# Kernel optimization log

Measured on AMD Instinct MI355X. Metric: run time of the kernel, lower is better.

## Reference

```python
import jax, jax.numpy as jnp
import numpy as np

B, BOUNDS, NRIM, K, UNITS = 4096, 512, 6, 4, 600
H_IN, DK_IN, DV_IN = 4, 64, 400
H_C, DK_C, DV_C = 4, 32, 100


def setup_inputs() -> dict:
    key = jax.random.key(0)
    ks = jax.random.split(key, 16)
    s = 0.02
    return {
        'inputs': jax.random.normal(ks[0], (B, BOUNDS + NRIM), jnp.float32),
        'hs': jax.random.normal(ks[1], (B, NRIM, UNITS), jnp.float32) * s,
        'cs': jax.random.normal(ks[2], (B, NRIM, UNITS), jnp.float32) * s,
        'Wk': jax.random.normal(ks[3], (BOUNDS, H_IN * DK_IN), jnp.float32) * s,
        'bk': jnp.zeros((H_IN * DK_IN,), jnp.float32),
        'Wv': jax.random.normal(ks[4], (BOUNDS, H_IN * DV_IN), jnp.float32) * s,
        'bv': jnp.zeros((H_IN * DV_IN,), jnp.float32),
        'Wq': jax.random.normal(ks[5], (NRIM, UNITS, H_IN * DK_IN), jnp.float32) * s,
        'lstm_k': jax.random.normal(ks[6], (NRIM, DV_IN, 4 * UNITS), jnp.float32) * s,
        'lstm_r': jax.random.normal(ks[7], (NRIM, UNITS, 4 * UNITS), jnp.float32) * s,
        'lstm_b': jnp.zeros((NRIM, 4 * UNITS), jnp.float32),
        'Wkc': jax.random.normal(ks[8], (NRIM, UNITS, H_C * DK_C), jnp.float32) * s,
        'Wvc': jax.random.normal(ks[9], (NRIM, UNITS, H_C * DV_C), jnp.float32) * s,
        'Wqc': jax.random.normal(ks[10], (NRIM, UNITS, H_C * DK_C), jnp.float32) * s,
        'Wout': jax.random.normal(ks[11], (NRIM, H_C * DV_C, UNITS), jnp.float32) * s,
    }


def _split_heads(t, n_heads, d_head):
    # [B, T, n_heads*d_head] -> [B, n_heads, T, d_head] (matches tf.split+stack)
    b, t_len = t.shape[0], t.shape[1]
    return t.reshape(b, t_len, n_heads, d_head).transpose(0, 2, 1, 3)


def reference(inputs, hs, cs, Wk, bk, Wv, bv, Wq, lstm_k, lstm_r, lstm_b, Wkc, Wvc, Wqc, Wout):
    x = inputs[:, :BOUNDS]                                   # [B, bounds]
    rim_dist = inputs[:, BOUNDS:BOUNDS + NRIM]               # [B, nRIM]

    # ---- input attention ----
    xx = jnp.stack([x, jnp.zeros_like(x)], axis=1)           # [B, 2, bounds]
    k_lay = xx @ Wk + bk                                     # [B, 2, H*dk]
    v_lay = xx @ Wv + bv                                     # [B, 2, H*dv]
    q_lay = jnp.einsum('bnu,nuo->bno', hs, Wq)               # grouped linear [B, nRIM, H*dq]
    kh = _split_heads(k_lay, H_IN, DK_IN)                    # [B, H, 2, dk]
    vh = _split_heads(v_lay, H_IN, DV_IN)                    # [B, H, 2, dv]
    qh = _split_heads(q_lay, H_IN, DK_IN)                    # [B, H, nRIM, dk]
    v2 = vh.mean(axis=1)                                     # [B, 2, dv]
    scores = jnp.einsum('bhnd,bhtd->bhnt', qh, kh) / np.sqrt(DK_IN).astype(np.float32)
    scores2 = scores.mean(axis=1)                            # [B, nRIM, 2]

    # top-k RIM selection mask from RIM_dist (use_attn=False path)
    _, idx = jax.lax.top_k(rim_dist, K)                      # [B, K]
    mask = jnp.zeros((inputs.shape[0], NRIM), inputs.dtype)
    mask = mask.at[jnp.arange(inputs.shape[0])[:, None], idx].set(1.0)[..., None]  # [B, nRIM, 1]

    probs = jax.nn.softmax(scores2, axis=-1)                 # dropout inactive (training=False)
    rnn_in = jnp.einsum('bnt,btv->bnv', probs, v2) * mask    # [B, nRIM, dv]

    # ---- grouped LSTM (keras gate order i,f,c,o) ----
    gates = (jnp.einsum('bnv,nvo->bno', rnn_in, lstm_k)
             + jnp.einsum('bnu,nuo->bno', hs, lstm_r) + lstm_b)  # [B, nRIM, 4*units]
    i, f, g, o = jnp.split(gates, 4, axis=-1)
    c_rnn = jax.nn.sigmoid(f) * cs + jax.nn.sigmoid(i) * jnp.tanh(g)
    h_rnn = jax.nn.sigmoid(o) * jnp.tanh(c_rnn)
    h_new = jax.lax.stop_gradient(h_rnn * (1.0 - mask)) + h_rnn * mask

    # ---- communication attention among RIMs ----
    kc = _split_heads(jnp.einsum('bnu,nuo->bno', h_new, Wkc), H_C, DK_C)  # [B, Hc, nRIM, dkc]
    vc = _split_heads(jnp.einsum('bnu,nuo->bno', h_new, Wvc), H_C, DV_C)
    qc = _split_heads(jnp.einsum('bnu,nuo->bno', h_new, Wqc), H_C, DK_C)
    sc = jnp.einsum('bhnd,bhmd->bhnm', qc, kc) / np.sqrt(DK_C).astype(np.float32)
    pc = jax.nn.softmax(sc, axis=-1) * mask[:, None, :, :]   # zero rows of inactive query RIMs
    ctx = jnp.einsum('bhnm,bhmv->bhnv', pc, vc)              # [B, Hc, nRIM, dvc]
    ctx = ctx.transpose(0, 2, 1, 3).reshape(inputs.shape[0], NRIM, H_C * DV_C)
    h_comm = jnp.einsum('bno,nou->bnu', ctx, Wout) + h_new   # grouped output proj + residual

    # ---- masked state update ----
    h_upd = h_comm * mask + hs * (1.0 - mask)
    c_upd = c_rnn * mask + cs * (1.0 - mask)
    out_state = h_upd.reshape(inputs.shape[0], UNITS * NRIM)
    return out_state, h_upd, c_upd
```

## Files before the change

### kernel.cpp

```cpp
#include <hip/hip_runtime.h>

namespace {
typedef unsigned short u16;
typedef __attribute__((ext_vector_type(8))) __bf16 bf16x8;
typedef __attribute__((ext_vector_type(4))) float f32x4;

constexpr long long kB  = 4096;
constexpr long long kOS = kB * 3600;
constexpr size_t kGAs = 4096ull * 1088;

constexpr size_t oWkvT  = 0;
constexpr size_t oWqT   = oWkvT  + 768ull*512*2;
constexpr size_t oWcomT = oWqT   + 6ull*256*640*2;
constexpr size_t oWoutT = oWcomT + 6ull*768*640*2;
constexpr size_t oLstmT = oWoutT + 6ull*640*448*2;
constexpr size_t oBp    = oLstmT + 6ull*2432*1024*2;
constexpr size_t oBkv   = oBp    + 6ull*2432*4;
constexpr size_t oMask  = oBkv   + 768*4;
constexpr size_t oArena = oMask  + 4096ull*6*4;
constexpr size_t oGA    = oArena;
constexpr size_t oKV    = oGA   + 6ull*kGAs*2;
constexpr size_t oXbf   = oKV   + 4096ull*768*2;
constexpr size_t oQlay  = oXbf;
constexpr size_t oCqv   = oArena;
constexpr size_t oCtx   = oCqv  + 4096ull*4608*2;
}

__device__ __forceinline__ u16 f2b(float f) {
  union { float f; unsigned u; } x; x.f = f;
  unsigned r = (x.u + 0x7fffu + ((x.u >> 16) & 1u)) >> 16;
  return (u16)r;
}
__device__ __forceinline__ float b2f(u16 u) {
  union { unsigned u; float f; } x; x.u = ((unsigned)u) << 16;
  return x.f;
}
__device__ __forceinline__ float sigmoidf_(float x) { return 1.f / (1.f + __expf(-x)); }
__device__ __forceinline__ float tanhf_(float x) {
  const float e = __expf(2.f * x);
  return 1.f - 2.f / (e + 1.f);
}

__device__ __forceinline__ void gload16(const void* g, void* l) {
  __builtin_amdgcn_global_load_lds((const __attribute__((address_space(1))) void*)g,
                                   (__attribute__((address_space(3))) void*)l, 16, 0, 0);
}

union FragU4 { uint4 u4; bf16x8 v; };

template<int MODE>
__global__ __launch_bounds__(256, 2) void gemm64(
    const u16* __restrict__ A, int lda, long strideA,
    const u16* __restrict__ Bt, long strideB, int Kpad,
    void* __restrict__ C, int ldc, int strideC,
    const float* __restrict__ bias, int strideBias,
    int N, int nks, int storeBf16, int nx, int swz,
    const float* __restrict__ cs, const float* __restrict__ mask,
    float* __restrict__ c_upd, float* __restrict__ h_upd, u16* __restrict__ hnbf,
    const float* __restrict__ hs_in, float* __restrict__ out_state)
{
  __shared__ __align__(16) u16 lds[2 * 16384];

  const int nwg = gridDim.x;
  const int orig = blockIdx.x;
  int wgid;
  {
    const int q = nwg >> 3, r = nwg & 7;
    const int xcd = orig & 7, bidx = orig >> 3;
    wgid = (xcd < r ? xcd * (q + 1) : r * (q + 1) + (xcd - r) * q) + bidx;
  }
  int mt, rim, xt;
  if (swz == 1) {
    const int g = wgid / 320, rem = wgid % 320;
    rim = g >> 1; mt = rem / 10; xt = (g & 1) * 10 + rem % 10;
    if (xt >= 19) return;
  } else {
    xt = wgid % nx;
    const int t2 = wgid / nx;
    mt = t2 & 31; rim = t2 >> 5;
  }
  const int m0 = mt * 128, n0 = xt * 128;

  A += (size_t)rim * strideA;
  Bt += (size_t)rim * strideB;
  if (bias) bias += (size_t)rim * strideBias;

  const int t = threadIdx.x;
  const int w = t >> 6, lane = t & 63;
  const int lrow = lane & 15, lk = lane >> 4;
  const int wr = w >> 1, wc = w & 1;

  f32x4 acc[4][4] = {};

  const u16* aS[4]; const u16* bS[4]; int cC[4];
#pragma unroll
  for (int i = 0; i < 4; ++i) {
    const int c = t + i * 256;
    const int row = c >> 3, slot = c & 7;
    cC[i] = c;
    aS[i] = A  + (size_t)(m0 + row) * lda  + ((slot ^ (row & 7)) << 3);
    bS[i] = Bt + (size_t)(n0 + row) * Kpad + ((slot ^ (row & 7)) << 3);
  }
  auto stage = [&](u16* dst) {
#pragma unroll
    for (int i = 0; i < 4; ++i) gload16(aS[i], dst + (size_t)cC[i] * 8);
#pragma unroll
    for (int i = 0; i < 4; ++i) gload16(bS[i], dst + 8192 + (size_t)cC[i] * 8);
#pragma unroll
    for (int i = 0; i < 4; ++i) { aS[i] += 64; bS[i] += 64; }
  };

  stage(lds);
  asm volatile("s_waitcnt vmcnt(0)" ::: "memory");
  __builtin_amdgcn_s_barrier();

  for (int s = 0; s < nks; ++s) {
    const bool more = (s + 1 < nks);
    if (more) stage(lds + ((s + 1) & 1) * 16384);
    __builtin_amdgcn_sched_barrier(0);
    const char* Ab = (const char*)(lds + (s & 1) * 16384);
    const char* Bb = Ab + 16384;
#pragma unroll
    for (int ks = 0; ks < 2; ++ks) {
      FragU4 af[4], bf4[4];
#pragma unroll
      for (int mf = 0; mf < 4; ++mf) {
        const int rr = wr * 64 + mf * 16 + lrow;
        af[mf].u4 = *(const uint4*)(Ab + rr * 128 + ((((ks << 2) | lk) ^ (rr & 7)) << 4));
      }
#pragma unroll
      for (int nf = 0; nf < 4; ++nf) {
        const int rr = wc * 64 + nf * 16 + lrow;
        bf4[nf].u4 = *(const uint4*)(Bb + rr * 128 + ((((ks << 2) | lk) ^ (rr & 7)) << 4));
      }
#pragma unroll
      for (int mf = 0; mf < 4; ++mf)
#pragma unroll
        for (int nf = 0; nf < 4; ++nf)
          acc[mf][nf] = __builtin_amdgcn_mfma_f32_16x16x32_bf16(af[mf].v, bf4[nf].v, acc[mf][nf], 0, 0, 0);
    }
    if (more) {
      asm volatile("s_waitcnt vmcnt(0)" ::: "memory");
      __builtin_amdgcn_s_barrier();
    }
  }

  if (MODE == 0) {
    float* Cf = (float*)C + (size_t)rim * strideC;
    u16*   Cu = (u16*)C + (size_t)rim * strideC;
#pragma unroll
    for (int mf = 0; mf < 4; ++mf)
#pragma unroll
      for (int r2 = 0; r2 < 4; ++r2) {
        const int m = m0 + wr * 64 + mf * 16 + 4 * lk + r2;
#pragma unroll
        for (int nf = 0; nf < 4; ++nf) {
          const int col = n0 + wc * 64 + nf * 16 + lrow;
          if (col < N) {
            float v = acc[mf][nf][r2];
            if (bias) v += bias[col];
            const size_t off = (size_t)m * ldc + col;
            if (storeBf16) Cu[off] = f2b(v); else Cf[off] = v;
          }
        }
      }
  } else if (MODE == 1) {
#pragma unroll
    for (int mf = 0; mf < 4; ++mf)
#pragma unroll
      for (int r2 = 0; r2 < 4; ++r2) {
        const int m = m0 + wr * 64 + mf * 16 + 4 * lk + r2;
        const float mk = mask[(size_t)m * 6 + rim];
#pragma unroll
        for (int nf = 0; nf < 4; ++nf) {
          const int col = n0 + wc * 64 + nf * 16 + lrow;
          if (col < 600) {
            const size_t off = (size_t)m * 3600 + rim * 600 + col;
            const float v = (mk != 0.f) ? (acc[mf][nf][r2] + h_upd[off]) : hs_in[off];
            h_upd[off] = v;
            out_state[off] = v;
          }
        }
      }
  } else {
    const int nb = n0 + wc * 64;
    const int u = ((nb >> 6) << 4) + lrow;
    if (u < 600) {
      const float b_i = bias[nb + lrow];
      const float b_f = bias[nb + 16 + lrow];
      const float b_g = bias[nb + 32 + lrow];
      const float b_o = bias[nb + 48 + lrow];
#pragma unroll
      for (int mf = 0; mf < 4; ++mf)
#pragma unroll
        for (int r2 = 0; r2 < 4; ++r2) {
          const int m = m0 + wr * 64 + mf * 16 + 4 * lk + r2;
          const float iv = acc[mf][0][r2] + b_i;
          const float fv = acc[mf][1][r2] + b_f;
          const float gv = acc[mf][2][r2] + b_g;
          const float ov = acc[mf][3][r2] + b_o;
          const size_t off = (size_t)m * 3600 + rim * 600 + u;
          const float cprev = cs[off];
          const float cv = sigmoidf_(fv) * cprev + sigmoidf_(iv) * tanhf_(gv);
          const float hv = sigmoidf_(ov) * tanhf_(cv);
          const float mk = mask[(size_t)m * 6 + rim];
          c_upd[off] = (mk != 0.f) ? cv : cprev;
          h_upd[off] = hv;
          hnbf[off]  = f2b(hv);
        }
    }
  }
}

__device__ void pack_wt_body(float (*tile)[65], int bx, int by, int rim,
    const float* __restrict__ i1, long s1, const float* __restrict__ i2, long s2,
    int K1, int Ktot, int ldin, int Nreal,
    u16* __restrict__ out, long so, int Kpad, int gateperm, int tid)
{
  i1 += (size_t)rim * s1;
  if (i2) i2 += (size_t)rim * s2;
  u16* o = out + (size_t)rim * so;
  const int n0 = bx * 64, k0 = by * 64;
  const int lane = tid & 63, qq = tid >> 6;
  const int n = n0 + lane;
  int col;
  if (gateperm) {
    const int g = (n >> 4) & 3, u = ((n >> 6) << 4) + (n & 15);
    col = (u < 600) ? g * 600 + u : -1;
  } else {
    col = (n < Nreal) ? n : -1;
  }
#pragma unroll
  for (int i = 0; i < 16; ++i) {
    const int kk = qq + 4 * i;
    const int k = k0 + kk;
    float v = 0.f;
    if (col >= 0) {
      if (k < K1) v = i1[(size_t)k * ldin + col];
      else if (k < Ktot) v = i2[(size_t)(k - K1) * ldin + col];
    }
    tile[kk][lane] = v;
  }
  __syncthreads();
#pragma unroll
  for (int i = 0; i < 16; ++i) {
    const int nn = qq + 4 * i;
    const int k = k0 + lane;
    if (k < Kpad) o[(size_t)(n0 + nn) * Kpad + k] = f2b(tile[lane][nn]);
  }
}

__global__ __launch_bounds__(256) void megapack_w(
    const float* __restrict__ Wk, const float* __restrict__ Wv,
    const float* __restrict__ Wkc, const float* __restrict__ Wqc, const float* __restrict__ Wvc,
    const float* __restrict__ Wq, const float* __restrict__ Wout,
    const float* __restrict__ lstm_k, const float* __restrict__ lstm_r,
    u16* __restrict__ WkvT, u16* __restrict__ WcomT, u16* __restrict__ WqT,
    u16* __restrict__ WoutT, u16* __restrict__ LstmT)
{
  __shared__ float tile[64][65];
  const int id = blockIdx.x, t = threadIdx.x;
  if (id < 3648) {
    const int bx = id % 38, by = (id / 38) % 16, bz = id / 608;
    pack_wt_body(tile, bx, by, bz, lstm_k, 400l*2400, lstm_r, 600l*2400,
                 400, 1000, 2400, 2400, LstmT, 2432l*1024, 1024, 1, t);
  } else if (id < 4068) {
    const int i2 = id - 3648;
    const int bx = i2 % 10, by = (i2 / 10) % 7, bz = i2 / 70;
    pack_wt_body(tile, bx, by, bz, Wout, 400l*600, nullptr, 0,
                 400, 400, 600, 600, WoutT, 640l*448, 448, 0, t);
  } else if (id < 4308) {
    const int i3 = id - 4068;
    const int bx = i3 % 4, by = (i3 / 4) % 10, bz = i3 / 40;
    pack_wt_body(tile, bx, by, bz, Wq, 600l*256, nullptr, 0,
                 600, 600, 256, 256, WqT, 256l*640, 640, 0, t);
  } else if (id < 4500) {
    const int e8 = ((id - 4308) * 256 + t) * 8;
    const int n = e8 >> 9, k0 = e8 & 511;
    u16 st[8];
#pragma unroll
    for (int j = 0; j < 8; ++j) {
      const int k = k0 + j;
      float v = 0.f;
      if (n < 256) v = Wk[(size_t)k * 256 + n];
      else if (n < 656) {
        const float* p = Wv + (size_t)k * 1600 + (n - 256);
        v = 0.25f * (p[0] + p[400] + p[800] + p[1200]);
      }
      st[j] = f2b(v);
    }
    *(uint4*)(WkvT + e8) = *(const uint4*)st;
  } else {
    const long long e8 = ((long long)(id - 4500) * 256 + t) * 8;
    const int rim = (int)(e8 / 491520);
    const int rem = (int)(e8 % 491520);
    const int n = rem / 640, k0 = rem % 640;
    u16 st[8];
#pragma unroll
    for (int j = 0; j < 8; ++j) {
      const int k = k0 + j;
      float v = 0.f;
      if (k < 600) {
        if (n < 128)      v = Wkc[(size_t)rim * 76800 + (size_t)k * 128 + n];
        else if (n < 256) v = Wqc[(size_t)rim * 76800 + (size_t)k * 128 + (n - 128)];
        else if (n < 656) v = Wvc[(size_t)rim * 240000 + (size_t)k * 400 + (n - 256)];
      }
      st[j] = f2b(v);
    }
    *(uint4*)(WcomT + e8) = *(const uint4*)st;
  }
}

__global__ __launch_bounds__(256) void megapack_act(
    const float* __restrict__ inputs, const float* __restrict__ hs,
    const float* __restrict__ lstm_b, const float* __restrict__ bk, const float* __restrict__ bv,
    u16* __restrict__ xbf, u16* __restrict__ gA, float* __restrict__ bp, float* __restrict__ bkv)
{
  __shared__ float row[3600];
  const int id = blockIdx.x, t = threadIdx.x;
  if (id < 4096) {
    const int b = id;
    for (int i = t; i < 3600; i += 256) row[i] = hs[(size_t)b * 3600 + i];
    __syncthreads();
    for (int c = t; c < 516; c += 256) {
      const int rim = c / 86;
      const int j = (c % 86) * 8;
      u16 v[8];
#pragma unroll
      for (int k = 0; k < 8; ++k) {
        const int col = j + k;
        v[k] = (col < 600) ? f2b(row[rim * 600 + col]) : (u16)0;
      }
      *(uint4*)(gA + (size_t)rim * kGAs + (size_t)b * 1088 + 400 + j) = *(const uint4*)v;
    }
  } else if (id < 5120) {
    const int e8 = ((id - 4096) * 256 + t) * 8;
    const int b = e8 >> 9, c0 = e8 & 511;
    const float* src = inputs + (size_t)b * 518 + c0;
    u16 st[8];
#pragma unroll
    for (int j = 0; j < 8; ++j) st[j] = f2b(src[j]);
    *(uint4*)(xbf + e8) = *(const uint4*)st;
  } else {
    const int tt = (id - 5120) * 256 + t;
    if (tt < 6 * 2432) {
      const int rim = tt / 2432, p = tt % 2432;
      const int g = (p >> 4) & 3, u = ((p >> 6) << 4) + (p & 15);
      bp[tt] = (u < 600) ? lstm_b[(size_t)rim * 2400 + g * 600 + u] : 0.f;
    }
    if (tt < 768) {
      float v = 0.f;
      if (tt < 256) v = bk[tt];
      else if (tt < 656) { const int j2 = tt - 256; v = 0.25f * (bv[j2] + bv[j2+400] + bv[j2+800] + bv[j2+1200]); }
      bkv[tt] = v;
    }
  }
}

__global__ __launch_bounds__(256) void score_kernel(
    const float* __restrict__ inputs, const u16* __restrict__ qlayb,
    const u16* __restrict__ kvb, const float* __restrict__ bk,
    const float* __restrict__ bkv,
    float* __restrict__ maskout, u16* __restrict__ gA)
{
  const int b = blockIdx.x;
  const int t = threadIdx.x;
  __shared__ float red[4][12];
  __shared__ float sprob[12];
  __shared__ float smask[6];

  const float k0v = b2f(kvb[(size_t)b * 768 + t]);
  const float bkv_ = bk[t];
  float part[12];
#pragma unroll
  for (int n = 0; n < 6; ++n) {
    const float q = b2f(qlayb[(size_t)b * 1536 + n * 256 + t]);
    part[2 * n]     = q * k0v;
    part[2 * n + 1] = q * bkv_;
  }
#pragma unroll
  for (int off = 32; off > 0; off >>= 1)
#pragma unroll
    for (int i = 0; i < 12; ++i)
      part[i] += __shfl_down(part[i], off);
  const int wave = t >> 6, lane = t & 63;
  if (lane == 0)
#pragma unroll
    for (int i = 0; i < 12; ++i) red[wave][i] = part[i];
  __syncthreads();
  if (t < 12) red[0][t] = (red[0][t] + red[1][t] + red[2][t] + red[3][t]) * (1.0f / 32.0f);
  __syncthreads();
  if (t < 6) {
    const float s0 = red[0][2 * t], s1 = red[0][2 * t + 1];
    const float mx = fmaxf(s0, s1);
    const float e0 = __expf(s0 - mx), e1 = __expf(s1 - mx);
    const float inv = 1.f / (e0 + e1);
    sprob[2 * t] = e0 * inv;
    sprob[2 * t + 1] = e1 * inv;
    const float* rd = inputs + (size_t)b * 518 + 512;
    const float mine = rd[t];
    int rank = 0;
#pragma unroll
    for (int j = 0; j < 6; ++j) {
      const float o = rd[j];
      rank += (o > mine) || (o == mine && j < t);
    }
    const float mk = (rank < 4) ? 1.f : 0.f;
    smask[t] = mk;
    maskout[(size_t)b * 6 + t] = mk;
  }
  __syncthreads();
  for (int c = t; c < 300; c += 256) {
    const int n = c / 50;
    const int v = (c % 50) * 8;
    const float p0 = sprob[2 * n], p1 = sprob[2 * n + 1], mk = smask[n];
    u16 st[8];
#pragma unroll
    for (int k = 0; k < 8; ++k)
      st[k] = f2b((p0 * b2f(kvb[(size_t)b * 768 + 256 + v + k]) + p1 * bkv[256 + v + k]) * mk);
    *reinterpret_cast<uint4*>(gA + (size_t)n * kGAs + (size_t)b * 1088 + v) =
        *reinterpret_cast<const uint4*>(st);
  }
}

__global__ __launch_bounds__(256) void comm_kernel(
    const u16* __restrict__ cqv, u16* __restrict__ ctx)
{
  const int b = blockIdx.x, t = threadIdx.x;
  __shared__ float skc[768], sqc[768], svc[2400];
  __shared__ float spc[4][6][6];
  for (int i = t * 4; i < 4608; i += 1024) {
    const ushort4 u4 = *reinterpret_cast<const ushort4*>(cqv + (size_t)b * 4608 + i);
    const u16 uu[4] = {u4.x, u4.y, u4.z, u4.w};
#pragma unroll
    for (int j = 0; j < 4; ++j) {
      const int ii = i + j;
      const int m = ii / 768, c = ii % 768;
      const float v = b2f(uu[j]);
      if (c < 128) skc[m * 128 + c] = v;
      else if (c < 256) sqc[m * 128 + (c - 128)] = v;
      else if (c < 656) svc[m * 400 + (c - 256)] = v;
    }
  }
  __syncthreads();
  if (t < 144) {
    const int h = t / 36, n = (t % 36) / 6, m = t % 6;
    float s = 0.f;
#pragma unroll
    for (int d = 0; d < 32; ++d) s += sqc[n * 128 + h * 32 + d] * skc[m * 128 + h * 32 + d];
    spc[h][n][m] = s * 0.17677669529663687f;
  }
  __syncthreads();
  if (t < 24) {
    const int h = t / 6, n = t % 6;
    float mx = -3.0e38f;
#pragma unroll
    for (int m = 0; m < 6; ++m) mx = fmaxf(mx, spc[h][n][m]);
    float e[6], sum = 0.f;
#pragma unroll
    for (int m = 0; m < 6; ++m) { e[m] = __expf(spc[h][n][m] - mx); sum += e[m]; }
    const float inv = 1.f / sum;
#pragma unroll
    for (int m = 0; m < 6; ++m) spc[h][n][m] = e[m] * inv;
  }
  __syncthreads();
  for (int base = t * 4; base < 2400; base += 1024) {
    const int n = base / 400, rr = base % 400, h = rr / 100, v = rr % 100;
    ushort4 st;
    float s0 = 0.f, s1 = 0.f, s2 = 0.f, s3 = 0.f;
#pragma unroll
    for (int m = 0; m < 6; ++m) {
      const float p = spc[h][n][m];
      const float* vm = &svc[m * 400 + h * 100 + v];
      s0 += p * vm[0]; s1 += p * vm[1]; s2 += p * vm[2]; s3 += p * vm[3];
    }
    st.x = f2b(s0); st.y = f2b(s1); st.z = f2b(s2); st.w = f2b(s3);
    *reinterpret_cast<ushort4*>(ctx + (size_t)b * 2400 + base) = st;
  }
}

extern "C" void kernel_launch(void* const* d_in, const int* in_sizes, int n_in,
                              void* d_out, int out_size, void* d_ws, size_t ws_size,
                              hipStream_t stream) {
  const float* inputs = (const float*)d_in[0];
  const float* hs     = (const float*)d_in[1];
  const float* cs     = (const float*)d_in[2];
  const float* Wk     = (const float*)d_in[3];
  const float* bk     = (const float*)d_in[4];
  const float* Wv     = (const float*)d_in[5];
  const float* bv     = (const float*)d_in[6];
  const float* Wq     = (const float*)d_in[7];
  const float* lstm_k = (const float*)d_in[8];
  const float* lstm_r = (const float*)d_in[9];
  const float* lstm_b = (const float*)d_in[10];
  const float* Wkc    = (const float*)d_in[11];
  const float* Wvc    = (const float*)d_in[12];
  const float* Wqc    = (const float*)d_in[13];
  const float* Wout   = (const float*)d_in[14];

  float* out = (float*)d_out;
  float* out_state = out;
  float* h_upd = out + kOS;
  float* c_upd = out + 2 * kOS;
  u16*   hnbf  = (u16*)d_out;

  char* wsb = (char*)d_ws;
  u16* WkvT  = (u16*)(wsb + oWkvT);
  u16* WqT   = (u16*)(wsb + oWqT);
  u16* WcomT = (u16*)(wsb + oWcomT);
  u16* WoutT = (u16*)(wsb + oWoutT);
  u16* LstmT = (u16*)(wsb + oLstmT);
  float* bp    = (float*)(wsb + oBp);
  float* bkv   = (float*)(wsb + oBkv);
  float* maskf = (float*)(wsb + oMask);
  u16* gA    = (u16*)(wsb + oGA);
  u16* kvb   = (u16*)(wsb + oKV);
  u16* xbf   = (u16*)(wsb + oXbf);
  u16* qlayb = (u16*)(wsb + oQlay);
  u16* cqvb  = (u16*)(wsb + oCqv);
  u16* ctxb  = (u16*)(wsb + oCtx);

  dim3 B256(256);

  megapack_w<<<5940, B256, 0, stream>>>(Wk, Wv, Wkc, Wqc, Wvc, Wq, Wout, lstm_k, lstm_r,
                                        WkvT, WcomT, WqT, WoutT, LstmT);
  megapack_act<<<5177, B256, 0, stream>>>(inputs, hs, lstm_b, bk, bv, xbf, gA, bp, bkv);

  gemm64<0><<<dim3(192), B256, 0, stream>>>(xbf, 512, 0, WkvT, 0, 512,
      kvb, 768, 0, bkv, 0, 656, 8, 1, 6, 0,
      nullptr, nullptr, nullptr, nullptr, nullptr, nullptr, nullptr);
  gemm64<0><<<dim3(384), B256, 0, stream>>>(gA + 400, 1088, (long)kGAs, WqT, 256l*640, 640,
      qlayb, 1536, 256, nullptr, 0, 256, 10, 1, 2, 0,
      nullptr, nullptr, nullptr, nullptr, nullptr, nullptr, nullptr);

  score_kernel<<<4096, B256, 0, stream>>>(inputs, qlayb, kvb, bk, bkv, maskf, gA);

  gemm64<2><<<dim3(3840), B256, 0, stream>>>(gA, 1088, (long)kGAs, LstmT, 2432l*1024, 1024,
      nullptr, 0, 0, bp, 2432, 2432, 16, 0, 0, 1,
      cs, maskf, c_upd, h_upd, hnbf, nullptr, nullptr);

  gemm64<0><<<dim3(1152), B256, 0, stream>>>(hnbf, 3600, 600, WcomT, 768l*640, 640,
      cqvb, 4608, 768, nullptr, 0, 656, 10, 1, 6, 0,
      nullptr, nullptr, nullptr, nullptr, nullptr, nullptr, nullptr);

  comm_kernel<<<4096, B256, 0, stream>>>(cqvb, ctxb);

  gemm64<1><<<dim3(960), B256, 0, stream>>>(ctxb, 2400, 400, WoutT, 640l*448, 448,
      nullptr, 0, 0, nullptr, 0, 600, 7, 0, 5, 0,
      nullptr, maskf, nullptr, h_upd, nullptr, hs, out_state);
}
```

Measured before the change: 578.5 us.

## Deepen GEMM LDS pipeline to four stages with half-size K slices

Reworks the shared bf16 GEMM mainloop from a double buffer of 64-wide K tiles to a four-slot ring of 32-wide K tiles, keeping three loads in flight. Partial vmcnt waits replace full drains, so each step waits only for its own stage. The LDS layout and swizzle are rebuilt to match, and every launch's K-step count is doubled. The goal is to hide global-load latency better. The cost is one barrier per 32-wide K step (twice as many barriers) and fewer MFMAs between them.

```diff
diff --git a/kernel.cpp b/kernel.cpp
--- a/kernel.cpp
+++ b/kernel.cpp
@@ -59,7 +59,7 @@
     float* __restrict__ c_upd, float* __restrict__ h_upd, u16* __restrict__ hnbf,
     const float* __restrict__ hs_in, float* __restrict__ out_state)
 {
-  __shared__ __align__(16) u16 lds[2 * 16384];
+  __shared__ __align__(16) u16 lds[4 * 8192];
 
   const int nwg = gridDim.x;
   const int orig = blockIdx.x;
@@ -92,57 +92,51 @@
 
   f32x4 acc[4][4] = {};
 
-  const u16* aS[4]; const u16* bS[4]; int cC[4];
-#pragma unroll
-  for (int i = 0; i < 4; ++i) {
+  const u16* aS[2]; const u16* bS[2];
+#pragma unroll
+  for (int i = 0; i < 2; ++i) {
     const int c = t + i * 256;
-    const int row = c >> 3, slot = c & 7;
-    cC[i] = c;
-    aS[i] = A  + (size_t)(m0 + row) * lda  + ((slot ^ (row & 7)) << 3);
-    bS[i] = Bt + (size_t)(n0 + row) * Kpad + ((slot ^ (row & 7)) << 3);
+    const int pr = c >> 3, su = (c & 7) ^ (pr & 7);
+    const int row = ((su >> 2) << 6) + pr;
+    const int kb = (su & 3) << 3;
+    aS[i] = A  + (size_t)(m0 + row) * lda  + kb;
+    bS[i] = Bt + (size_t)(n0 + row) * Kpad + kb;
   }
   auto stage = [&](u16* dst) {
-#pragma unroll
-    for (int i = 0; i < 4; ++i) gload16(aS[i], dst + (size_t)cC[i] * 8);
-#pragma unroll
-    for (int i = 0; i < 4; ++i) gload16(bS[i], dst + 8192 + (size_t)cC[i] * 8);
-#pragma unroll
-    for (int i = 0; i < 4; ++i) { aS[i] += 64; bS[i] += 64; }
+    gload16(aS[0], dst + (size_t)t * 8);
+    gload16(aS[1], dst + (size_t)(t + 256) * 8);
+    gload16(bS[0], dst + 4096 + (size_t)t * 8);
+    gload16(bS[1], dst + 4096 + (size_t)(t + 256) * 8);
+    aS[0] += 32; aS[1] += 32; bS[0] += 32; bS[1] += 32;
   };
 
-  stage(lds);
-  asm volatile("s_waitcnt vmcnt(0)" ::: "memory");
-  __builtin_amdgcn_s_barrier();
+  const int npro = nks < 3 ? nks : 3;
+  for (int i = 0; i < npro; ++i) stage(lds + i * 8192);
+
+  const int slA = (((wr << 2) | lk) ^ (lrow & 7)) << 4;
+  const int slB = (((wc << 2) | lk) ^ (lrow & 7)) << 4;
 
   for (int s = 0; s < nks; ++s) {
-    const bool more = (s + 1 < nks);
-    if (more) stage(lds + ((s + 1) & 1) * 16384);
+    if (s + 2 < nks)       asm volatile("s_waitcnt vmcnt(8)" ::: "memory");
+    else if (s + 2 == nks) asm volatile("s_waitcnt vmcnt(4)" ::: "memory");
+    else                   asm volatile("s_waitcnt vmcnt(0)" ::: "memory");
+    __builtin_amdgcn_s_barrier();
+    if (s + 3 < nks) stage(lds + ((s + 3) & 3) * 8192);
     __builtin_amdgcn_sched_barrier(0);
-    const char* Ab = (const char*)(lds + (s & 1) * 16384);
-    const char* Bb = Ab + 16384;
-#pragma unroll
-    for (int ks = 0; ks < 2; ++ks) {
-      FragU4 af[4], bf4[4];
-#pragma unroll
-      for (int mf = 0; mf < 4; ++mf) {
-        const int rr = wr * 64 + mf * 16 + lrow;
-        af[mf].u4 = *(const uint4*)(Ab + rr * 128 + ((((ks << 2) | lk) ^ (rr & 7)) << 4));
-      }
-#pragma unroll
-      for (int nf = 0; nf < 4; ++nf) {
-        const int rr = wc * 64 + nf * 16 + lrow;
-        bf4[nf].u4 = *(const uint4*)(Bb + rr * 128 + ((((ks << 2) | lk) ^ (rr & 7)) << 4));
-      }
-#pragma unroll
-      for (int mf = 0; mf < 4; ++mf)
-#pragma unroll
-        for (int nf = 0; nf < 4; ++nf)
-          acc[mf][nf] = __builtin_amdgcn_mfma_f32_16x16x32_bf16(af[mf].v, bf4[nf].v, acc[mf][nf], 0, 0, 0);
-    }
-    if (more) {
-      asm volatile("s_waitcnt vmcnt(0)" ::: "memory");
-      __builtin_amdgcn_s_barrier();
-    }
+    const char* Ab = (const char*)(lds + (s & 3) * 8192);
+    const char* Bb = Ab + 8192;
+    FragU4 af[4], bf4[4];
+#pragma unroll
+    for (int mf = 0; mf < 4; ++mf)
+      af[mf].u4 = *(const uint4*)(Ab + (mf * 16 + lrow) * 128 + slA);
+#pragma unroll
+    for (int nf = 0; nf < 4; ++nf)
+      bf4[nf].u4 = *(const uint4*)(Bb + (nf * 16 + lrow) * 128 + slB);
+#pragma unroll
+    for (int mf = 0; mf < 4; ++mf)
+#pragma unroll
+      for (int nf = 0; nf < 4; ++nf)
+        acc[mf][nf] = __builtin_amdgcn_mfma_f32_16x16x32_bf16(af[mf].v, bf4[nf].v, acc[mf][nf], 0, 0, 0);
   }
 
   if (MODE == 0) {
@@ -527,25 +521,25 @@
   megapack_act<<<5177, B256, 0, stream>>>(inputs, hs, lstm_b, bk, bv, xbf, gA, bp, bkv);
 
   gemm64<0><<<dim3(192), B256, 0, stream>>>(xbf, 512, 0, WkvT, 0, 512,
-      kvb, 768, 0, bkv, 0, 656, 8, 1, 6, 0,
+      kvb, 768, 0, bkv, 0, 656, 16, 1, 6, 0,
       nullptr, nullptr, nullptr, nullptr, nullptr, nullptr, nullptr);
   gemm64<0><<<dim3(384), B256, 0, stream>>>(gA + 400, 1088, (long)kGAs, WqT, 256l*640, 640,
-      qlayb, 1536, 256, nullptr, 0, 256, 10, 1, 2, 0,
+      qlayb, 1536, 256, nullptr, 0, 256, 20, 1, 2, 0,
       nullptr, nullptr, nullptr, nullptr, nullptr, nullptr, nullptr);
 
   score_kernel<<<4096, B256, 0, stream>>>(inputs, qlayb, kvb, bk, bkv, maskf, gA);
 
   gemm64<2><<<dim3(3840), B256, 0, stream>>>(gA, 1088, (long)kGAs, LstmT, 2432l*1024, 1024,
-      nullptr, 0, 0, bp, 2432, 2432, 16, 0, 0, 1,
+      nullptr, 0, 0, bp, 2432, 2432, 32, 0, 0, 1,
       cs, maskf, c_upd, h_upd, hnbf, nullptr, nullptr);
 
   gemm64<0><<<dim3(1152), B256, 0, stream>>>(hnbf, 3600, 600, WcomT, 768l*640, 640,
-      cqvb, 4608, 768, nullptr, 0, 656, 10, 1, 6, 0,
+      cqvb, 4608, 768, nullptr, 0, 656, 20, 1, 6, 0,
       nullptr, nullptr, nullptr, nullptr, nullptr, nullptr, nullptr);
 
   comm_kernel<<<4096, B256, 0, stream>>>(cqvb, ctxb);
 
   gemm64<1><<<dim3(960), B256, 0, stream>>>(ctxb, 2400, 400, WoutT, 640l*448, 448,
-      nullptr, 0, 0, nullptr, 0, 600, 7, 0, 5, 0,
+      nullptr, 0, 0, nullptr, 0, 600, 14, 0, 5, 0,
       nullptr, maskf, nullptr, h_upd, nullptr, hs, out_state);
 }
```

Measured after the change: 622.5 us. 7.6% more time.

## Make GEMM kernel persistent with contiguous tile ranges and pad hidden-state buffer

Applied to the files above, without the earlier changes.

The GEMM kernel becomes persistent. Each workgroup now walks a contiguous range of tiles (rim-major, m-tile innermost), and the large GEMMs launch with 512 workgroups instead of thousands, with a barrier between tiles. The bf16 hidden-state buffer gets a padded row stride of 3648, with the tail zeroed in the activation pack kernel, so the comm GEMM no longer reads past row ends into the next row. This aims to cut launch and tail-wave overhead and improve weight reuse within each workgroup, at the cost of possible load imbalance and no overlap of prologue and epilogue across tiles.

```diff
diff --git a/kernel.cpp b/kernel.cpp
--- a/kernel.cpp
+++ b/kernel.cpp
@@ -8,6 +8,7 @@
 constexpr long long kB  = 4096;
 constexpr long long kOS = kB * 3600;
 constexpr size_t kGAs = 4096ull * 1088;
+constexpr int kHnS = 3648;
 
 constexpr size_t oWkvT  = 0;
 constexpr size_t oWqT   = oWkvT  + 768ull*512*2;
@@ -54,161 +55,162 @@
     const u16* __restrict__ Bt, long strideB, int Kpad,
     void* __restrict__ C, int ldc, int strideC,
     const float* __restrict__ bias, int strideBias,
-    int N, int nks, int storeBf16, int nx, int swz,
+    int N, int nks, int storeBf16, int nx, int ntiles,
     const float* __restrict__ cs, const float* __restrict__ mask,
     float* __restrict__ c_upd, float* __restrict__ h_upd, u16* __restrict__ hnbf,
     const float* __restrict__ hs_in, float* __restrict__ out_state)
 {
   __shared__ __align__(16) u16 lds[2 * 16384];
 
-  const int nwg = gridDim.x;
+  const int P = gridDim.x;
   const int orig = blockIdx.x;
   int wgid;
   {
-    const int q = nwg >> 3, r = nwg & 7;
+    const int q = P >> 3, r = P & 7;
     const int xcd = orig & 7, bidx = orig >> 3;
     wgid = (xcd < r ? xcd * (q + 1) : r * (q + 1) + (xcd - r) * q) + bidx;
   }
-  int mt, rim, xt;
-  if (swz == 1) {
-    const int g = wgid / 320, rem = wgid % 320;
-    rim = g >> 1; mt = rem / 10; xt = (g & 1) * 10 + rem % 10;
-    if (xt >= 19) return;
-  } else {
-    xt = wgid % nx;
-    const int t2 = wgid / nx;
-    mt = t2 & 31; rim = t2 >> 5;
-  }
-  const int m0 = mt * 128, n0 = xt * 128;
-
-  A += (size_t)rim * strideA;
-  Bt += (size_t)rim * strideB;
-  if (bias) bias += (size_t)rim * strideBias;
+  const int cbase = ntiles / P, cextra = ntiles % P;
+  int ti = wgid * cbase + (wgid < cextra ? wgid : cextra);
+  const int tend = ti + cbase + (wgid < cextra ? 1 : 0);
 
   const int t = threadIdx.x;
   const int w = t >> 6, lane = t & 63;
   const int lrow = lane & 15, lk = lane >> 4;
   const int wr = w >> 1, wc = w & 1;
 
-  f32x4 acc[4][4] = {};
-
-  const u16* aS[4]; const u16* bS[4]; int cC[4];
-#pragma unroll
-  for (int i = 0; i < 4; ++i) {
-    const int c = t + i * 256;
-    const int row = c >> 3, slot = c & 7;
-    cC[i] = c;
-    aS[i] = A  + (size_t)(m0 + row) * lda  + ((slot ^ (row & 7)) << 3);
-    bS[i] = Bt + (size_t)(n0 + row) * Kpad + ((slot ^ (row & 7)) << 3);
-  }
-  auto stage = [&](u16* dst) {
-#pragma unroll
-    for (int i = 0; i < 4; ++i) gload16(aS[i], dst + (size_t)cC[i] * 8);
-#pragma unroll
-    for (int i = 0; i < 4; ++i) gload16(bS[i], dst + 8192 + (size_t)cC[i] * 8);
-#pragma unroll
-    for (int i = 0; i < 4; ++i) { aS[i] += 64; bS[i] += 64; }
-  };
-
-  stage(lds);
-  asm volatile("s_waitcnt vmcnt(0)" ::: "memory");
-  __builtin_amdgcn_s_barrier();
-
-  for (int s = 0; s < nks; ++s) {
-    const bool more = (s + 1 < nks);
-    if (more) stage(lds + ((s + 1) & 1) * 16384);
-    __builtin_amdgcn_sched_barrier(0);
-    const char* Ab = (const char*)(lds + (s & 1) * 16384);
-    const char* Bb = Ab + 16384;
-#pragma unroll
-    for (int ks = 0; ks < 2; ++ks) {
-      FragU4 af[4], bf4[4];
-#pragma unroll
-      for (int mf = 0; mf < 4; ++mf) {
-        const int rr = wr * 64 + mf * 16 + lrow;
-        af[mf].u4 = *(const uint4*)(Ab + rr * 128 + ((((ks << 2) | lk) ^ (rr & 7)) << 4));
+  for (; ti < tend; ++ti) {
+    const int mt = ti & 31;
+    const int g = ti >> 5;
+    const int xt = g % nx;
+    const int rim = g / nx;
+    const int m0 = mt * 128, n0 = xt * 128;
+
+    const u16* At = A + (size_t)rim * strideA;
+    const u16* Bp = Bt + (size_t)rim * strideB;
+    const float* bip = bias ? bias + (size_t)rim * strideBias : nullptr;
+
+    f32x4 acc[4][4] = {};
+
+    const u16* aS[4]; const u16* bS[4]; int cC[4];
+#pragma unroll
+    for (int i = 0; i < 4; ++i) {
+      const int c = t + i * 256;
+      const int row = c >> 3, slot = c & 7;
+      cC[i] = c;
+      aS[i] = At + (size_t)(m0 + row) * lda  + ((slot ^ (row & 7)) << 3);
+      bS[i] = Bp + (size_t)(n0 + row) * Kpad + ((slot ^ (row & 7)) << 3);
+    }
+    auto stage = [&](u16* dst) {
+#pragma unroll
+      for (int i = 0; i < 4; ++i) gload16(aS[i], dst + (size_t)cC[i] * 8);
+#pragma unroll
+      for (int i = 0; i < 4; ++i) gload16(bS[i], dst + 8192 + (size_t)cC[i] * 8);
+#pragma unroll
+      for (int i = 0; i < 4; ++i) { aS[i] += 64; bS[i] += 64; }
+    };
+
+    stage(lds);
+    asm volatile("s_waitcnt vmcnt(0)" ::: "memory");
+    __builtin_amdgcn_s_barrier();
+
+    for (int s = 0; s < nks; ++s) {
+      const bool more = (s + 1 < nks);
+      if (more) stage(lds + ((s + 1) & 1) * 16384);
+      __builtin_amdgcn_sched_barrier(0);
+      const char* Ab = (const char*)(lds + (s & 1) * 16384);
+      const char* Bb = Ab + 16384;
+#pragma unroll
+      for (int ks = 0; ks < 2; ++ks) {
+        FragU4 af[4], bf4[4];
+#pragma unroll
+        for (int mf = 0; mf < 4; ++mf) {
+          const int rr = wr * 64 + mf * 16 + lrow;
+          af[mf].u4 = *(const uint4*)(Ab + rr * 128 + ((((ks << 2) | lk) ^ (rr & 7)) << 4));
+        }
+#pragma unroll
+        for (int nf = 0; nf < 4; ++nf) {
+          const int rr = wc * 64 + nf * 16 + lrow;
+          bf4[nf].u4 = *(const uint4*)(Bb + rr * 128 + ((((ks << 2) | lk) ^ (rr & 7)) << 4));
+        }
+#pragma unroll
+        for (int mf = 0; mf < 4; ++mf)
+#pragma unroll
+          for (int nf = 0; nf < 4; ++nf)
+            acc[mf][nf] = __builtin_amdgcn_mfma_f32_16x16x32_bf16(af[mf].v, bf4[nf].v, acc[mf][nf], 0, 0, 0);
       }
-#pragma unroll
-      for (int nf = 0; nf < 4; ++nf) {
-        const int rr = wc * 64 + nf * 16 + lrow;
-        bf4[nf].u4 = *(const uint4*)(Bb + rr * 128 + ((((ks << 2) | lk) ^ (rr & 7)) << 4));
+      if (more) {
+        asm volatile("s_waitcnt vmcnt(0)" ::: "memory");
+        __builtin_amdgcn_s_barrier();
       }
+    }
+
+    if (MODE == 0) {
+      float* Cf = (float*)C + (size_t)rim * strideC;
+      u16*   Cu = (u16*)C + (size_t)rim * strideC;
 #pragma unroll
       for (int mf = 0; mf < 4; ++mf)
 #pragma unroll
-        for (int nf = 0; nf < 4; ++nf)
-          acc[mf][nf] = __builtin_amdgcn_mfma_f32_16x16x32_bf16(af[mf].v, bf4[nf].v, acc[mf][nf], 0, 0, 0);
-    }
-    if (more) {
-      asm volatile("s_waitcnt vmcnt(0)" ::: "memory");
-      __builtin_amdgcn_s_barrier();
-    }
-  }
-
-  if (MODE == 0) {
-    float* Cf = (float*)C + (size_t)rim * strideC;
-    u16*   Cu = (u16*)C + (size_t)rim * strideC;
-#pragma unroll
-    for (int mf = 0; mf < 4; ++mf)
-#pragma unroll
-      for (int r2 = 0; r2 < 4; ++r2) {
-        const int m = m0 + wr * 64 + mf * 16 + 4 * lk + r2;
-#pragma unroll
-        for (int nf = 0; nf < 4; ++nf) {
-          const int col = n0 + wc * 64 + nf * 16 + lrow;
-          if (col < N) {
-            float v = acc[mf][nf][r2];
-            if (bias) v += bias[col];
-            const size_t off = (size_t)m * ldc + col;
-            if (storeBf16) Cu[off] = f2b(v); else Cf[off] = v;
+        for (int r2 = 0; r2 < 4; ++r2) {
+          const int m = m0 + wr * 64 + mf * 16 + 4 * lk + r2;
+#pragma unroll
+          for (int nf = 0; nf < 4; ++nf) {
+            const int col = n0 + wc * 64 + nf * 16 + lrow;
+            if (col < N) {
+              float v = acc[mf][nf][r2];
+              if (bip) v += bip[col];
+              const size_t off = (size_t)m * ldc + col;
+              if (storeBf16) Cu[off] = f2b(v); else Cf[off] = v;
+            }
           }
         }
-      }
-  } else if (MODE == 1) {
-#pragma unroll
-    for (int mf = 0; mf < 4; ++mf)
-#pragma unroll
-      for (int r2 = 0; r2 < 4; ++r2) {
-        const int m = m0 + wr * 64 + mf * 16 + 4 * lk + r2;
-        const float mk = mask[(size_t)m * 6 + rim];
-#pragma unroll
-        for (int nf = 0; nf < 4; ++nf) {
-          const int col = n0 + wc * 64 + nf * 16 + lrow;
-          if (col < 600) {
-            const size_t off = (size_t)m * 3600 + rim * 600 + col;
-            const float v = (mk != 0.f) ? (acc[mf][nf][r2] + h_upd[off]) : hs_in[off];
-            h_upd[off] = v;
-            out_state[off] = v;
+    } else if (MODE == 1) {
+#pragma unroll
+      for (int mf = 0; mf < 4; ++mf)
+#pragma unroll
+        for (int r2 = 0; r2 < 4; ++r2) {
+          const int m = m0 + wr * 64 + mf * 16 + 4 * lk + r2;
+          const float mk = mask[(size_t)m * 6 + rim];
+#pragma unroll
+          for (int nf = 0; nf < 4; ++nf) {
+            const int col = n0 + wc * 64 + nf * 16 + lrow;
+            if (col < 600) {
+              const size_t off = (size_t)m * 3600 + rim * 600 + col;
+              const float v = (mk != 0.f) ? (acc[mf][nf][r2] + h_upd[off]) : hs_in[off];
+              h_upd[off] = v;
+              out_state[off] = v;
+            }
           }
         }
+    } else {
+      const int nb = n0 + wc * 64;
+      const int u = ((nb >> 6) << 4) + lrow;
+      if (u < 600) {
+        const float b_i = bip[nb + lrow];
+        const float b_f = bip[nb + 16 + lrow];
+        const float b_g = bip[nb + 32 + lrow];
+        const float b_o = bip[nb + 48 + lrow];
+#pragma unroll
+        for (int mf = 0; mf < 4; ++mf)
+#pragma unroll
+          for (int r2 = 0; r2 < 4; ++r2) {
+            const int m = m0 + wr * 64 + mf * 16 + 4 * lk + r2;
+            const float iv = acc[mf][0][r2] + b_i;
+            const float fv = acc[mf][1][r2] + b_f;
+            const float gv = acc[mf][2][r2] + b_g;
+            const float ov = acc[mf][3][r2] + b_o;
+            const size_t off = (size_t)m * 3600 + rim * 600 + u;
+            const float cprev = cs[off];
+            const float cv = sigmoidf_(fv) * cprev + sigmoidf_(iv) * tanhf_(gv);
+            const float hv = sigmoidf_(ov) * tanhf_(cv);
+            const float mk = mask[(size_t)m * 6 + rim];
+            c_upd[off] = (mk != 0.f) ? cv : cprev;
+            h_upd[off] = hv;
+            hnbf[(size_t)m * kHnS + rim * 600 + u] = f2b(hv);
+          }
       }
-  } else {
-    const int nb = n0 + wc * 64;
-    const int u = ((nb >> 6) << 4) + lrow;
-    if (u < 600) {
-      const float b_i = bias[nb + lrow];
-      const float b_f = bias[nb + 16 + lrow];
-      const float b_g = bias[nb + 32 + lrow];
-      const float b_o = bias[nb + 48 + lrow];
-#pragma unroll
-      for (int mf = 0; mf < 4; ++mf)
-#pragma unroll
-        for (int r2 = 0; r2 < 4; ++r2) {
-          const int m = m0 + wr * 64 + mf * 16 + 4 * lk + r2;
-          const float iv = acc[mf][0][r2] + b_i;
-          const float fv = acc[mf][1][r2] + b_f;
-          const float gv = acc[mf][2][r2] + b_g;
-          const float ov = acc[mf][3][r2] + b_o;
-          const size_t off = (size_t)m * 3600 + rim * 600 + u;
-          const float cprev = cs[off];
-          const float cv = sigmoidf_(fv) * cprev + sigmoidf_(iv) * tanhf_(gv);
-          const float hv = sigmoidf_(ov) * tanhf_(cv);
-          const float mk = mask[(size_t)m * 6 + rim];
-          c_upd[off] = (mk != 0.f) ? cv : cprev;
-          h_upd[off] = hv;
-          hnbf[off]  = f2b(hv);
-        }
-    }
+    }
+    __syncthreads();
   }
 }
 
@@ -314,7 +316,8 @@
 __global__ __launch_bounds__(256) void megapack_act(
     const float* __restrict__ inputs, const float* __restrict__ hs,
     const float* __restrict__ lstm_b, const float* __restrict__ bk, const float* __restrict__ bv,
-    u16* __restrict__ xbf, u16* __restrict__ gA, float* __restrict__ bp, float* __restrict__ bkv)
+    u16* __restrict__ xbf, u16* __restrict__ gA, float* __restrict__ bp, float* __restrict__ bkv,
+    u16* __restrict__ hnbf)
 {
   __shared__ float row[3600];
   const int id = blockIdx.x, t = threadIdx.x;
@@ -332,6 +335,10 @@
         v[k] = (col < 600) ? f2b(row[rim * 600 + col]) : (u16)0;
       }
       *(uint4*)(gA + (size_t)rim * kGAs + (size_t)b * 1088 + 400 + j) = *(const uint4*)v;
+    }
+    if (t < 6) {
+      u16 z[8] = {0,0,0,0,0,0,0,0};
+      *(uint4*)(hnbf + (size_t)b * kHnS + 3600 + t * 8) = *(const uint4*)z;
     }
   } else if (id < 5120) {
     const int e8 = ((id - 4096) * 256 + t) * 8;
@@ -524,28 +531,28 @@
 
   megapack_w<<<5940, B256, 0, stream>>>(Wk, Wv, Wkc, Wqc, Wvc, Wq, Wout, lstm_k, lstm_r,
                                         WkvT, WcomT, WqT, WoutT, LstmT);
-  megapack_act<<<5177, B256, 0, stream>>>(inputs, hs, lstm_b, bk, bv, xbf, gA, bp, bkv);
+  megapack_act<<<5177, B256, 0, stream>>>(inputs, hs, lstm_b, bk, bv, xbf, gA, bp, bkv, hnbf);
 
   gemm64<0><<<dim3(192), B256, 0, stream>>>(xbf, 512, 0, WkvT, 0, 512,
-      kvb, 768, 0, bkv, 0, 656, 8, 1, 6, 0,
+      kvb, 768, 0, bkv, 0, 656, 8, 1, 6, 192,
       nullptr, nullptr, nullptr, nullptr, nullptr, nullptr, nullptr);
   gemm64<0><<<dim3(384), B256, 0, stream>>>(gA + 400, 1088, (long)kGAs, WqT, 256l*640, 640,
-      qlayb, 1536, 256, nullptr, 0, 256, 10, 1, 2, 0,
+      qlayb, 1536, 256, nullptr, 0, 256, 10, 1, 2, 384,
       nullptr, nullptr, nullptr, nullptr, nullptr, nullptr, nullptr);
 
   score_kernel<<<4096, B256, 0, stream>>>(inputs, qlayb, kvb, bk, bkv, maskf, gA);
 
-  gemm64<2><<<dim3(3840), B256, 0, stream>>>(gA, 1088, (long)kGAs, LstmT, 2432l*1024, 1024,
-      nullptr, 0, 0, bp, 2432, 2432, 16, 0, 0, 1,
+  gemm64<2><<<dim3(512), B256, 0, stream>>>(gA, 1088, (long)kGAs, LstmT, 2432l*1024, 1024,
+      nullptr, 0, 0, bp, 2432, 2432, 16, 0, 19, 3648,
       cs, maskf, c_upd, h_upd, hnbf, nullptr, nullptr);
 
-  gemm64<0><<<dim3(1152), B256, 0, stream>>>(hnbf, 3600, 600, WcomT, 768l*640, 640,
-      cqvb, 4608, 768, nullptr, 0, 656, 10, 1, 6, 0,
+  gemm64<0><<<dim3(512), B256, 0, stream>>>(hnbf, kHnS, 600, WcomT, 768l*640, 640,
+      cqvb, 4608, 768, nullptr, 0, 656, 10, 1, 6, 1152,
       nullptr, nullptr, nullptr, nullptr, nullptr, nullptr, nullptr);
 
   comm_kernel<<<4096, B256, 0, stream>>>(cqvb, ctxb);
 
-  gemm64<1><<<dim3(960), B256, 0, stream>>>(ctxb, 2400, 400, WoutT, 640l*448, 448,
-      nullptr, 0, 0, nullptr, 0, 600, 7, 0, 5, 0,
+  gemm64<1><<<dim3(512), B256, 0, stream>>>(ctxb, 2400, 400, WoutT, 640l*448, 448,
+      nullptr, 0, 0, nullptr, 0, 600, 7, 0, 5, 960,
       nullptr, maskf, nullptr, h_upd, nullptr, hs, out_state);
 }
```

Measured after the change: 618.5 us. 6.9% more time.
